# Kernel tuning notes

Hardware: AMD Instinct MI355X
Metric: run time of the kernel (lower is better)

## Reference

```python
import jax, jax.numpy as jnp
import numpy as np

B = 256      # graphs per batch
N = 512      # nodes per graph
FEAT = 64    # num_features
H = 64       # nhid
DEG = 16     # avg degree
RATIO = 0.5  # pooling_ratio
E = B * N * DEG


def setup_inputs() -> dict:
    key = jax.random.key(0)
    ks = jax.random.split(key, 12)
    # edges constructed within each graph via offsets
    src_loc = jax.random.randint(ks[0], (B, N * DEG), 0, N)
    dst_loc = jax.random.randint(ks[1], (B, N * DEG), 0, N)
    offs = (jnp.arange(B) * N)[:, None]
    edge_src = (src_loc + offs).reshape(-1).astype(jnp.int32)
    edge_dst = (dst_loc + offs).reshape(-1).astype(jnp.int32)
    batch = jnp.repeat(jnp.arange(B, dtype=jnp.int32), N)
    x = jax.random.normal(ks[2], (B * N, FEAT), dtype=jnp.float32)
    edge_attr = jax.random.uniform(ks[3], (E,), dtype=jnp.float32) + 0.1
    s1 = 1.0 / np.sqrt(FEAT)
    s2 = 1.0 / np.sqrt(H)
    return {
        "x": x,
        "edge_attr": edge_attr,
        "W1": jax.random.normal(ks[4], (FEAT, H), jnp.float32) * s1,
        "b1": jnp.zeros((H,), jnp.float32),
        "Wp1": jax.random.normal(ks[5], (H, 1), jnp.float32) * s2,
        "bp1": jnp.zeros((1,), jnp.float32),
        "W2": jax.random.normal(ks[6], (H, H), jnp.float32) * s2,
        "b2": jnp.zeros((H,), jnp.float32),
        "Wp2": jax.random.normal(ks[7], (H, 1), jnp.float32) * s2,
        "bp2": jnp.zeros((1,), jnp.float32),
        "edge_src": edge_src,
        "edge_dst": edge_dst,
        "batch": batch,
    }


def gcn_conv(x, W, b, src, dst, ew, n):
    """PyG GCNConv: sym-normalized weighted adjacency + self-loops (weight 1)."""
    h = x @ W                                   # [n, out]
    deg = jnp.zeros((n,), x.dtype).at[dst].add(ew) + 1.0  # self-loop adds 1
    dinv = jax.lax.rsqrt(deg)
    coef = dinv[dst] * ew * dinv[src]           # [E]
    out = jnp.zeros_like(h).at[dst].add(coef[:, None] * h[src])
    out = out + h * (1.0 / deg)[:, None]        # self-loop term: deg^-0.5 * 1 * deg^-0.5
    return out + b


def sag_pool(x, src, dst, ew, Wp, bp, n_per):
    """SAGPool: score = GCNConv(x)->1, per-graph top-k, gate by tanh(score),
    filter edges (dropped edges represented by zero weight)."""
    n = x.shape[0]
    score = gcn_conv(x, Wp, bp, src, dst, ew, n)[:, 0]   # [n]
    k = int(np.ceil(RATIO * n_per))
    _, idx = jax.lax.top_k(score.reshape(B, n_per), k)   # [B, k] local indices
    perm = (idx + (jnp.arange(B) * n_per)[:, None]).reshape(-1)
    xn = x[perm] * jnp.tanh(score[perm])[:, None]        # [B*k, H]
    newid = jnp.full((n,), -1, jnp.int32).at[perm].set(
        jnp.arange(B * k, dtype=jnp.int32))
    ns, nd = newid[src], newid[dst]
    valid = (ns >= 0) & (nd >= 0)
    ew2 = jnp.where(valid, ew, 0.0)
    ns = jnp.where(valid, ns, 0)
    nd = jnp.where(valid, nd, 0)
    return xn, ns, nd, ew2, k


def readout(x, k):
    """[gmp || gap] per graph; each graph has exactly k nodes, contiguous."""
    xg = x.reshape(B, k, -1)
    return jnp.concatenate([xg.max(axis=1), xg.mean(axis=1)], axis=1)  # [B, 2H]


def reference(x, edge_attr, W1, b1, Wp1, bp1, W2, b2, Wp2, bp2,
              edge_src, edge_dst, batch):
    n0 = x.shape[0]
    h = jax.nn.relu(gcn_conv(x, W1, b1, edge_src, edge_dst, edge_attr, n0))
    h, s1, d1, w1e, k1 = sag_pool(h, edge_src, edge_dst, edge_attr, Wp1, bp1, N)
    x1 = readout(h, k1)
    h = jax.nn.relu(gcn_conv(h, W2, b2, s1, d1, w1e, B * k1))
    h, _, _, _, k2 = sag_pool(h, s1, d1, w1e, Wp2, bp2, k1)
    x2 = readout(h, k2)
    return (x1 + x2) / 2.0
```

## Files before the change

### kernel.cpp

```cpp
#include <hip/hip_runtime.h>
#include <math.h>

#define BG   256
#define NN   512
#define EPG  (NN * 16)
#define NE   (BG * EPG)
#define N0   (BG * NN)
#define K1   256
#define N1_  (BG * K1)
#define K2   128
#define N2_  (BG * K2)

__device__ __forceinline__ float4 f4fma(float s, float4 a, float4 c) {
    c.x = fmaf(s, a.x, c.x); c.y = fmaf(s, a.y, c.y);
    c.z = fmaf(s, a.z, c.z); c.w = fmaf(s, a.w, c.w);
    return c;
}

template <int NPG, bool REMAP>
__global__ __launch_bounds__(512)
void stage_head_kernel(const int* __restrict__ esrc, const int* __restrict__ edst,
                       const float* __restrict__ eatt, const int* __restrict__ nid,
                       int2* __restrict__ pairs, int* __restrict__ rowstart,
                       int* __restrict__ rowcnt, float* __restrict__ dinv,
                       const float4* __restrict__ X4, const float4* __restrict__ W4,
                       float4* __restrict__ Y4, int nrows, int mmb) {
    __shared__ __align__(16) char smem[52224];
    if ((int)blockIdx.x < BG) {
        int2*  lpair = (int2*)smem;
        int*   cnt   = (int*)(smem + 32768);
        float* wsum  = (float*)(smem + 32768) + NPG;
        int*   scn   = (int*)(smem + 32768) + 2 * NPG;
        float* sdinv = (float*)(smem + 32768) + 3 * NPG;
        int*   wtot  = (int*)(smem + 32768) + 4 * NPG;
        int g = blockIdx.x;
        int e0 = g * EPG, nbase = g * NPG;
        for (int ii = threadIdx.x; ii < NPG; ii += 512) { cnt[ii] = 0; wsum[ii] = 0.f; }
        __syncthreads();
        const int4*   edst4 = (const int4*)(edst + e0);
        const int4*   esrc4 = (const int4*)(esrc + e0);
        const float4* eatt4 = (const float4*)(eatt + e0);
        int ed[16]; int es[16]; float ea[16];
#pragma unroll
        for (int c = 0; c < 4; ++c) {
            int ch = threadIdx.x + c * 512;
            int4   dd = edst4[ch];
            int4   ss = esrc4[ch];
            float4 ww = eatt4[ch];
            ed[c * 4 + 0] = dd.x; ed[c * 4 + 1] = dd.y; ed[c * 4 + 2] = dd.z; ed[c * 4 + 3] = dd.w;
            es[c * 4 + 0] = ss.x; es[c * 4 + 1] = ss.y; es[c * 4 + 2] = ss.z; es[c * 4 + 3] = ss.w;
            ea[c * 4 + 0] = ww.x; ea[c * 4 + 1] = ww.y; ea[c * 4 + 2] = ww.z; ea[c * 4 + 3] = ww.w;
        }
        if (REMAP) {
#pragma unroll
            for (int j = 0; j < 16; ++j) { ed[j] = nid[ed[j]]; es[j] = nid[es[j]]; }
        }
#pragma unroll
        for (int j = 0; j < 16; ++j) {
            bool valid = !REMAP || (ed[j] >= 0 && es[j] >= 0);
            if (valid) {
                int dl = ed[j] - nbase;
                atomicAdd(&cnt[dl], 1);
                atomicAdd(&wsum[dl], ea[j]);
            }
        }
        __syncthreads();
        int i = threadIdx.x;
        int lane = i & 63, wvid = i >> 6;
        int xval = (i < NPG) ? cnt[i] : 0;
        int xs = xval;
#pragma unroll
        for (int off = 1; off < 64; off <<= 1) {
            int v = __shfl_up(xs, off, 64);
            if (lane >= off) xs += v;
        }
        if (lane == 63) wtot[wvid] = xs;
        __syncthreads();
        int woff = 0, total = 0;
#pragma unroll
        for (int t = 0; t < 8; ++t) {
            int wt = wtot[t];
            if (t < wvid) woff += wt;
            total += wt;
        }
        xs += woff;
        if (i < NPG) {
            int st = xs - xval;
            rowstart[nbase + i] = e0 + st;
            rowcnt[nbase + i]   = xval;
            float di = rsqrtf(wsum[i] + 1.0f);
            dinv[nbase + i] = di;
            sdinv[i] = di;
            scn[i] = st;
        }
        __syncthreads();
        int slots[16]; float cf[16];
#pragma unroll
        for (int j = 0; j < 16; ++j) {
            bool valid = !REMAP || (ed[j] >= 0 && es[j] >= 0);
            slots[j] = -1;
            if (valid) {
                int dl = ed[j] - nbase, sl = es[j] - nbase;
                cf[j] = sdinv[dl] * ea[j] * sdinv[sl];
                slots[j] = atomicAdd(&scn[dl], 1);
            }
        }
#pragma unroll
        for (int j = 0; j < 16; ++j)
            if (slots[j] >= 0 && slots[j] < 4096)
                lpair[slots[j]] = make_int2(es[j] - nbase, __float_as_int(cf[j]));
        __syncthreads();
        int n0 = total < 4096 ? total : 4096;
        for (int k = threadIdx.x; k < n0; k += 512) pairs[e0 + k] = lpair[k];
        __syncthreads();
        if (total > 4096) {
#pragma unroll
            for (int j = 0; j < 16; ++j)
                if (slots[j] >= 4096)
                    lpair[slots[j] - 4096] = make_int2(es[j] - nbase, __float_as_int(cf[j]));
            __syncthreads();
            int n1 = total - 4096;
            for (int k = threadIdx.x; k < n1; k += 512) pairs[e0 + 4096 + k] = lpair[k];
        }
    } else {
        float (*sW)[68] = (float (*)[68])smem;
        int p = threadIdx.x >> 8;
        int t = threadIdx.x & 255;
        float (*sX)[68] = (float (*)[68])(smem + 17408 + p * 17408);
#pragma unroll
        for (int u = 0; u < 2; ++u) {
            int idx = threadIdx.x + u * 512;
            int r = idx >> 4, c4 = idx & 15;
            *(float4*)&sW[r][c4 * 4] = W4[idx];
        }
        int mb = blockIdx.x - BG;
        int ntiles = nrows >> 6;
        int rg = t >> 4, cg = t & 15;
        for (int tile = mb * 2 + p; tile < ntiles; tile += mmb * 2) {
            __syncthreads();
            int row0 = tile << 6;
#pragma unroll
            for (int u = 0; u < 4; ++u) {
                int idx = t + u * 256;
                int r = idx >> 4, c4 = idx & 15;
                *(float4*)&sX[r][c4 * 4] = X4[(size_t)(row0 + r) * 16 + c4];
            }
            __syncthreads();
            float4 acc0 = make_float4(0.f, 0.f, 0.f, 0.f);
            float4 acc1 = acc0, acc2 = acc0, acc3 = acc0;
#pragma unroll
            for (int k4 = 0; k4 < 16; ++k4) {
                float4 xv0 = *(const float4*)&sX[rg * 4 + 0][k4 * 4];
                float4 xv1 = *(const float4*)&sX[rg * 4 + 1][k4 * 4];
                float4 xv2 = *(const float4*)&sX[rg * 4 + 2][k4 * 4];
                float4 xv3 = *(const float4*)&sX[rg * 4 + 3][k4 * 4];
                float4 wv0 = *(const float4*)&sW[k4 * 4 + 0][cg * 4];
                float4 wv1 = *(const float4*)&sW[k4 * 4 + 1][cg * 4];
                float4 wv2 = *(const float4*)&sW[k4 * 4 + 2][cg * 4];
                float4 wv3 = *(const float4*)&sW[k4 * 4 + 3][cg * 4];
                acc0 = f4fma(xv0.x, wv0, acc0); acc0 = f4fma(xv0.y, wv1, acc0);
                acc0 = f4fma(xv0.z, wv2, acc0); acc0 = f4fma(xv0.w, wv3, acc0);
                acc1 = f4fma(xv1.x, wv0, acc1); acc1 = f4fma(xv1.y, wv1, acc1);
                acc1 = f4fma(xv1.z, wv2, acc1); acc1 = f4fma(xv1.w, wv3, acc1);
                acc2 = f4fma(xv2.x, wv0, acc2); acc2 = f4fma(xv2.y, wv1, acc2);
                acc2 = f4fma(xv2.z, wv2, acc2); acc2 = f4fma(xv2.w, wv3, acc2);
                acc3 = f4fma(xv3.x, wv0, acc3); acc3 = f4fma(xv3.y, wv1, acc3);
                acc3 = f4fma(xv3.z, wv2, acc3); acc3 = f4fma(xv3.w, wv3, acc3);
            }
            size_t ob = (size_t)(row0 + rg * 4) * 16 + cg;
            Y4[ob]      = acc0;
            Y4[ob + 16] = acc1;
            Y4[ob + 32] = acc2;
            Y4[ob + 48] = acc3;
        }
    }
}

template <int NPG, int K, bool FINAL>
__global__ __launch_bounds__(512)
void tail_kernel(const float4* __restrict__ hx4, const int2* __restrict__ pairs,
                 const int* __restrict__ rowstart, const int* __restrict__ rowcnt,
                 const float* __restrict__ dinv, const float4* __restrict__ b4,
                 const float4* __restrict__ wp4, const float* __restrict__ bp,
                 int* __restrict__ nid, float4* __restrict__ xn4,
                 float* __restrict__ xr, const float* __restrict__ x1r,
                 float* __restrict__ out) {
    constexpr int PASSES = NPG / 32;
    constexpr int SH_A  = NPG * 68;
    constexpr int SH_UN = 4096;
    __shared__ __align__(16) float smem[SH_A + SH_UN + 2 * NPG + 64 + 64];
    float*  shx  = smem;
    int*    perm = (int*)(smem + SH_A);
    float*  shp  = smem + SH_A + NPG;
    float4* smx  = (float4*)(smem + SH_A);
    float4* ssm  = (float4*)(smem + SH_A + 2048);
    float*  ssc  = smem + SH_A + SH_UN;
    int*    rnk  = (int*)(smem + SH_A + SH_UN + NPG);
    float*  sbw  = smem + SH_A + SH_UN + 2 * NPG;
    int*    hist = (int*)(smem + SH_A + SH_UN + 2 * NPG + 64);

    int g = blockIdx.x, nbase = g * NPG;
    int t = threadIdx.x;
    int lane16 = t & 15, sub = (t >> 4) & 3, wv = t >> 6, lane = t & 63;

    for (int i = t; i < NPG * 16; i += 512) {
        int r = i >> 4, c4 = i & 15;
        *(float4*)&shx[r * 68 + c4 * 4] = hx4[(size_t)nbase * 16 + i];
    }
    if (t < 64) { sbw[t] = ((const float*)b4)[t]; hist[t] = 0; }
    __syncthreads();
    for (int i = t; i < NPG; i += 512) {
        int c = min(rowcnt[nbase + i], 63);
        atomicAdd(&hist[c], 1);
    }
    __syncthreads();
    if (t < 64) {
        int v = hist[t], s = v;
#pragma unroll
        for (int off = 1; off < 64; off <<= 1) {
            int u = __shfl_up(s, off, 64);
            if (lane >= off) s += u;
        }
        hist[t] = s - v;
    }
    __syncthreads();
    for (int i = t; i < NPG; i += 512) {
        int c = min(rowcnt[nbase + i], 63);
        int pos = atomicAdd(&hist[c], 1);
        perm[pos] = i;
    }
    __syncthreads();
    int idx = wv * 64 + lane;
    float4 acc[16];
    int nl = 0;
    if (idx < NPG) {
        nl = perm[idx];
        int st = rowstart[nbase + nl], cn = rowcnt[nbase + nl];
        float di = dinv[nbase + nl], dii = di * di;
#pragma unroll
        for (int c = 0; c < 16; ++c) {
            float4 xv = *(const float4*)&shx[nl * 68 + c * 4];
            acc[c].x = fmaf(xv.x, dii, sbw[c * 4 + 0]);
            acc[c].y = fmaf(xv.y, dii, sbw[c * 4 + 1]);
            acc[c].z = fmaf(xv.z, dii, sbw[c * 4 + 2]);
            acc[c].w = fmaf(xv.w, dii, sbw[c * 4 + 3]);
        }
        int2 pc = (cn > 0) ? pairs[st] : make_int2(0, 0);
        for (int j = 0; j < cn; ++j) {
            int2 pn = (j + 1 < cn) ? pairs[st + j + 1] : make_int2(0, 0);
            float cf = __int_as_float(pc.y);
            int   s  = pc.x;
#pragma unroll
            for (int c = 0; c < 16; ++c)
                acc[c] = f4fma(cf, *(const float4*)&shx[s * 68 + c * 4], acc[c]);
            pc = pn;
        }
#pragma unroll
        for (int c = 0; c < 16; ++c) {
            acc[c].x = fmaxf(acc[c].x, 0.f); acc[c].y = fmaxf(acc[c].y, 0.f);
            acc[c].z = fmaxf(acc[c].z, 0.f); acc[c].w = fmaxf(acc[c].w, 0.f);
        }
    }
    __syncthreads();
    if (idx < NPG) {
#pragma unroll
        for (int c = 0; c < 16; ++c)
            *(float4*)&shx[nl * 68 + c * 4] = acc[c];
    }
    __syncthreads();
    float4 w4 = wp4[lane16];
#pragma unroll
    for (int p = 0; p < PASSES; ++p) {
        int n2 = p * 32 + wv * 4 + sub;
        float4 a = *(const float4*)&shx[n2 * 68 + lane16 * 4];
        float tt = a.x * w4.x + a.y * w4.y + a.z * w4.z + a.w * w4.w;
        tt += __shfl_xor(tt, 1, 64); tt += __shfl_xor(tt, 2, 64);
        tt += __shfl_xor(tt, 4, 64); tt += __shfl_xor(tt, 8, 64);
        if (lane16 == 0) shp[n2] = tt;
    }
    __syncthreads();
    if (t < NPG) {
        int i = perm[t];
        int st = rowstart[nbase + i], cn = rowcnt[nbase + i];
        float di = dinv[nbase + i];
        float a = fmaf(shp[i], di * di, bp[0]);
        for (int j = 0; j < cn; ++j) {
            int2 pr = pairs[st + j];
            a = fmaf(__int_as_float(pr.y), shp[pr.x], a);
        }
        ssc[i] = a;
    }
    __syncthreads();
    for (int i = t; i < NPG; i += 512) {
        float si = ssc[i];
        int rank = 0;
        for (int j = 0; j < NPG; ++j) {
            float sj = ssc[j];
            rank += (sj > si) || (sj == si && j < i);
        }
        rnk[i] = rank;
        if (!FINAL) nid[nbase + i] = (rank < K) ? (g * K + rank) : -1;
    }
    __syncthreads();
    float4 mx = make_float4(-3.402823466e38f, -3.402823466e38f, -3.402823466e38f, -3.402823466e38f);
    float4 sm = make_float4(0.f, 0.f, 0.f, 0.f);
#pragma unroll
    for (int p = 0; p < PASSES; ++p) {
        int n2 = p * 32 + wv * 4 + sub;
        int r = rnk[n2];
        if (r < K) {
            float gt = tanhf(ssc[n2]);
            float4 v = *(const float4*)&shx[n2 * 68 + lane16 * 4];
            v.x *= gt; v.y *= gt; v.z *= gt; v.w *= gt;
            if (!FINAL) xn4[((size_t)g * K + r) * 16 + lane16] = v;
            mx.x = fmaxf(mx.x, v.x); mx.y = fmaxf(mx.y, v.y);
            mx.z = fmaxf(mx.z, v.z); mx.w = fmaxf(mx.w, v.w);
            sm.x += v.x; sm.y += v.y; sm.z += v.z; sm.w += v.w;
        }
    }
    int grp = t >> 4;
    __syncthreads();
    smx[grp * 16 + lane16] = mx;
    ssm[grp * 16 + lane16] = sm;
    __syncthreads();
    if (grp == 0) {
#pragma unroll
        for (int u = 1; u < 32; ++u) {
            float4 a = smx[u * 16 + lane16], b = ssm[u * 16 + lane16];
            mx.x = fmaxf(mx.x, a.x); mx.y = fmaxf(mx.y, a.y);
            mx.z = fmaxf(mx.z, a.z); mx.w = fmaxf(mx.w, a.w);
            sm.x += b.x; sm.y += b.y; sm.z += b.z; sm.w += b.w;
        }
        float invK = 1.f / K;
        int c = lane16 * 4;
        float mr[4] = {mx.x, mx.y, mx.z, mx.w};
        float ar[4] = {sm.x * invK, sm.y * invK, sm.z * invK, sm.w * invK};
#pragma unroll
        for (int u = 0; u < 4; ++u) {
            if (FINAL) {
                out[g * 128 + c + u]      = 0.5f * (x1r[g * 128 + c + u]      + mr[u]);
                out[g * 128 + 64 + c + u] = 0.5f * (x1r[g * 128 + 64 + c + u] + ar[u]);
            } else {
                xr[g * 128 + c + u]      = mr[u];
                xr[g * 128 + 64 + c + u] = ar[u];
            }
        }
    }
}

extern "C" void kernel_launch(void* const* d_in, const int* in_sizes, int n_in,
                              void* d_out, int out_size, void* d_ws, size_t ws_size,
                              hipStream_t stream) {
    const float* x    = (const float*)d_in[0];
    const float* eatt = (const float*)d_in[1];
    const float* W1   = (const float*)d_in[2];
    const float* b1   = (const float*)d_in[3];
    const float* Wp1  = (const float*)d_in[4];
    const float* bp1  = (const float*)d_in[5];
    const float* W2   = (const float*)d_in[6];
    const float* b2   = (const float*)d_in[7];
    const float* Wp2  = (const float*)d_in[8];
    const float* bp2  = (const float*)d_in[9];
    const int*   esrc = (const int*)d_in[10];
    const int*   edst = (const int*)d_in[11];
    float* out = (float*)d_out;

    float* ws = (float*)d_ws;
    size_t o = 0;
    float* A    = ws + o; o += (size_t)N0 * 64;
    float* xn1  = ws + o; o += (size_t)N1_ * 64;
    int2*  prs  = (int2*)(ws + o); o += (size_t)NE * 2;
    int*   rst  = (int*)(ws + o); o += N0;
    int*   rcn  = (int*)(ws + o); o += N0;
    float* dinv = ws + o; o += N0;
    int*   nid  = (int*)(ws + o); o += N0;
    float* x1r  = ws + o; o += BG * 128;

    float* hx1 = A;
    float* hx2 = A;

    stage_head_kernel<NN, false><<<BG + 512, 512, 0, stream>>>(
        esrc, edst, eatt, nullptr, prs, rst, rcn, dinv,
        (const float4*)x, (const float4*)W1, (float4*)hx1, N0, 512);
    tail_kernel<NN, K1, false><<<BG, 512, 0, stream>>>(
        (const float4*)hx1, prs, rst, rcn, dinv, (const float4*)b1,
        (const float4*)Wp1, bp1, nid, (float4*)xn1, x1r, nullptr, nullptr);
    stage_head_kernel<K1, true><<<BG + 256, 512, 0, stream>>>(
        esrc, edst, eatt, nid, prs, rst, rcn, dinv,
        (const float4*)xn1, (const float4*)W2, (float4*)hx2, N1_, 256);
    tail_kernel<K1, K2, true><<<BG, 512, 0, stream>>>(
        (const float4*)hx2, prs, rst, rcn, dinv, (const float4*)b2,
        (const float4*)Wp2, bp2, nullptr, nullptr, nullptr, x1r, out);
}
```

Baseline: 224.5 us.

## Double tail kernel block to 1024 threads, splitting aggregation and ranking work

The tail kernel now runs 1024 threads per graph. The neighbor aggregation splits each node's 64 features across 2 or 4 threads, which cuts per-thread accumulator registers. The O(N^2) top-k rank computation is split across thread partitions using float4 reads, with the partial ranks combined by shared atomics. A deeper edge-pair prefetch is added. The cost is more threads competing for LDS and more barriers, with half the threads idle in the score and readout phases.

```diff
diff --git a/kernel.cpp b/kernel.cpp
--- a/kernel.cpp
+++ b/kernel.cpp
@@ -177,7 +177,7 @@
 }
 
 template <int NPG, int K, bool FINAL>
-__global__ __launch_bounds__(512)
+__global__ __launch_bounds__(1024)
 void tail_kernel(const float4* __restrict__ hx4, const int2* __restrict__ pairs,
                  const int* __restrict__ rowstart, const int* __restrict__ rowcnt,
                  const float* __restrict__ dinv, const float4* __restrict__ b4,
@@ -186,6 +186,11 @@
                  float* __restrict__ xr, const float* __restrict__ x1r,
                  float* __restrict__ out) {
     constexpr int PASSES = NPG / 32;
+    constexpr int LPN = 1024 / NPG;
+    constexpr int LOG_LPN = (LPN == 2) ? 1 : 2;
+    constexpr int QF = 16 / LPN;
+    constexpr int RLOG = (NPG == 512) ? 9 : 8;
+    constexpr int RCH = NPG * NPG / 1024;
     constexpr int SH_A  = NPG * 68;
     constexpr int SH_UN = 4096;
     __shared__ __align__(16) float smem[SH_A + SH_UN + 2 * NPG + 64 + 64];
@@ -201,15 +206,16 @@
 
     int g = blockIdx.x, nbase = g * NPG;
     int t = threadIdx.x;
-    int lane16 = t & 15, sub = (t >> 4) & 3, wv = t >> 6, lane = t & 63;
-
-    for (int i = t; i < NPG * 16; i += 512) {
+    int lane16 = t & 15, lane = t & 63;
+
+    for (int i = t; i < NPG * 16; i += 1024) {
         int r = i >> 4, c4 = i & 15;
         *(float4*)&shx[r * 68 + c4 * 4] = hx4[(size_t)nbase * 16 + i];
     }
     if (t < 64) { sbw[t] = ((const float*)b4)[t]; hist[t] = 0; }
-    __syncthreads();
-    for (int i = t; i < NPG; i += 512) {
+    for (int i = t; i < NPG; i += 1024) rnk[i] = 0;
+    __syncthreads();
+    for (int i = t; i < NPG; i += 1024) {
         int c = min(rowcnt[nbase + i], 63);
         atomicAdd(&hist[c], 1);
     }
@@ -224,59 +230,62 @@
         hist[t] = s - v;
     }
     __syncthreads();
-    for (int i = t; i < NPG; i += 512) {
+    for (int i = t; i < NPG; i += 1024) {
         int c = min(rowcnt[nbase + i], 63);
         int pos = atomicAdd(&hist[c], 1);
         perm[pos] = i;
     }
     __syncthreads();
-    int idx = wv * 64 + lane;
-    float4 acc[16];
-    int nl = 0;
-    if (idx < NPG) {
-        nl = perm[idx];
+    {
+        int idx2 = t >> LOG_LPN;
+        int half = t & (LPN - 1);
+        int nl = perm[idx2];
         int st = rowstart[nbase + nl], cn = rowcnt[nbase + nl];
         float di = dinv[nbase + nl], dii = di * di;
-#pragma unroll
-        for (int c = 0; c < 16; ++c) {
-            float4 xv = *(const float4*)&shx[nl * 68 + c * 4];
-            acc[c].x = fmaf(xv.x, dii, sbw[c * 4 + 0]);
-            acc[c].y = fmaf(xv.y, dii, sbw[c * 4 + 1]);
-            acc[c].z = fmaf(xv.z, dii, sbw[c * 4 + 2]);
-            acc[c].w = fmaf(xv.w, dii, sbw[c * 4 + 3]);
-        }
-        int2 pc = (cn > 0) ? pairs[st] : make_int2(0, 0);
+        int fb = half * QF;
+        float4 acc[QF];
+#pragma unroll
+        for (int c = 0; c < QF; ++c) {
+            float4 xv = *(const float4*)&shx[nl * 68 + (fb + c) * 4];
+            acc[c].x = fmaf(xv.x, dii, sbw[(fb + c) * 4 + 0]);
+            acc[c].y = fmaf(xv.y, dii, sbw[(fb + c) * 4 + 1]);
+            acc[c].z = fmaf(xv.z, dii, sbw[(fb + c) * 4 + 2]);
+            acc[c].w = fmaf(xv.w, dii, sbw[(fb + c) * 4 + 3]);
+        }
+        int2 p0 = (cn > 0) ? pairs[st] : make_int2(0, 0);
+        int2 p1 = (cn > 1) ? pairs[st + 1] : make_int2(0, 0);
         for (int j = 0; j < cn; ++j) {
-            int2 pn = (j + 1 < cn) ? pairs[st + j + 1] : make_int2(0, 0);
-            float cf = __int_as_float(pc.y);
-            int   s  = pc.x;
-#pragma unroll
-            for (int c = 0; c < 16; ++c)
-                acc[c] = f4fma(cf, *(const float4*)&shx[s * 68 + c * 4], acc[c]);
-            pc = pn;
-        }
-#pragma unroll
-        for (int c = 0; c < 16; ++c) {
+            int2 p2 = (j + 2 < cn) ? pairs[st + j + 2] : make_int2(0, 0);
+            float cf = __int_as_float(p0.y);
+            int   s  = p0.x;
+#pragma unroll
+            for (int c = 0; c < QF; ++c)
+                acc[c] = f4fma(cf, *(const float4*)&shx[s * 68 + (fb + c) * 4], acc[c]);
+            p0 = p1; p1 = p2;
+        }
+#pragma unroll
+        for (int c = 0; c < QF; ++c) {
             acc[c].x = fmaxf(acc[c].x, 0.f); acc[c].y = fmaxf(acc[c].y, 0.f);
             acc[c].z = fmaxf(acc[c].z, 0.f); acc[c].w = fmaxf(acc[c].w, 0.f);
         }
-    }
-    __syncthreads();
-    if (idx < NPG) {
-#pragma unroll
-        for (int c = 0; c < 16; ++c)
-            *(float4*)&shx[nl * 68 + c * 4] = acc[c];
-    }
-    __syncthreads();
-    float4 w4 = wp4[lane16];
-#pragma unroll
-    for (int p = 0; p < PASSES; ++p) {
-        int n2 = p * 32 + wv * 4 + sub;
-        float4 a = *(const float4*)&shx[n2 * 68 + lane16 * 4];
-        float tt = a.x * w4.x + a.y * w4.y + a.z * w4.z + a.w * w4.w;
-        tt += __shfl_xor(tt, 1, 64); tt += __shfl_xor(tt, 2, 64);
-        tt += __shfl_xor(tt, 4, 64); tt += __shfl_xor(tt, 8, 64);
-        if (lane16 == 0) shp[n2] = tt;
+        __syncthreads();
+#pragma unroll
+        for (int c = 0; c < QF; ++c)
+            *(float4*)&shx[nl * 68 + (fb + c) * 4] = acc[c];
+    }
+    __syncthreads();
+    if (t < 512) {
+        int wv8 = t >> 6, sub4 = (t >> 4) & 3;
+        float4 w4 = wp4[lane16];
+#pragma unroll
+        for (int p = 0; p < PASSES; ++p) {
+            int n2 = p * 32 + wv8 * 4 + sub4;
+            float4 a = *(const float4*)&shx[n2 * 68 + lane16 * 4];
+            float tt = a.x * w4.x + a.y * w4.y + a.z * w4.z + a.w * w4.w;
+            tt += __shfl_xor(tt, 1, 64); tt += __shfl_xor(tt, 2, 64);
+            tt += __shfl_xor(tt, 4, 64); tt += __shfl_xor(tt, 8, 64);
+            if (lane16 == 0) shp[n2] = tt;
+        }
     }
     __syncthreads();
     if (t < NPG) {
@@ -284,44 +293,60 @@
         int st = rowstart[nbase + i], cn = rowcnt[nbase + i];
         float di = dinv[nbase + i];
         float a = fmaf(shp[i], di * di, bp[0]);
+        int2 q0 = (cn > 0) ? pairs[st] : make_int2(0, 0);
+        int2 q1 = (cn > 1) ? pairs[st + 1] : make_int2(0, 0);
         for (int j = 0; j < cn; ++j) {
-            int2 pr = pairs[st + j];
-            a = fmaf(__int_as_float(pr.y), shp[pr.x], a);
+            int2 q2 = (j + 2 < cn) ? pairs[st + j + 2] : make_int2(0, 0);
+            a = fmaf(__int_as_float(q0.y), shp[q0.x], a);
+            q0 = q1; q1 = q2;
         }
         ssc[i] = a;
     }
     __syncthreads();
-    for (int i = t; i < NPG; i += 512) {
+    {
+        int part = t >> RLOG;
+        int i = t & (NPG - 1);
         float si = ssc[i];
+        int j0 = part * RCH;
         int rank = 0;
-        for (int j = 0; j < NPG; ++j) {
-            float sj = ssc[j];
-            rank += (sj > si) || (sj == si && j < i);
-        }
-        rnk[i] = rank;
-        if (!FINAL) nid[nbase + i] = (rank < K) ? (g * K + rank) : -1;
-    }
-    __syncthreads();
+        for (int j = j0; j < j0 + RCH; j += 4) {
+            float4 sj = *(const float4*)&ssc[j];
+            rank += (sj.x > si) || (sj.x == si && j     < i);
+            rank += (sj.y > si) || (sj.y == si && j + 1 < i);
+            rank += (sj.z > si) || (sj.z == si && j + 2 < i);
+            rank += (sj.w > si) || (sj.w == si && j + 3 < i);
+        }
+        atomicAdd(&rnk[i], rank);
+    }
+    __syncthreads();
+    if (!FINAL)
+        for (int i = t; i < NPG; i += 1024)
+            nid[nbase + i] = (rnk[i] < K) ? (g * K + rnk[i]) : -1;
     float4 mx = make_float4(-3.402823466e38f, -3.402823466e38f, -3.402823466e38f, -3.402823466e38f);
     float4 sm = make_float4(0.f, 0.f, 0.f, 0.f);
-#pragma unroll
-    for (int p = 0; p < PASSES; ++p) {
-        int n2 = p * 32 + wv * 4 + sub;
-        int r = rnk[n2];
-        if (r < K) {
-            float gt = tanhf(ssc[n2]);
-            float4 v = *(const float4*)&shx[n2 * 68 + lane16 * 4];
-            v.x *= gt; v.y *= gt; v.z *= gt; v.w *= gt;
-            if (!FINAL) xn4[((size_t)g * K + r) * 16 + lane16] = v;
-            mx.x = fmaxf(mx.x, v.x); mx.y = fmaxf(mx.y, v.y);
-            mx.z = fmaxf(mx.z, v.z); mx.w = fmaxf(mx.w, v.w);
-            sm.x += v.x; sm.y += v.y; sm.z += v.z; sm.w += v.w;
+    if (t < 512) {
+        int wv8 = t >> 6, sub4 = (t >> 4) & 3;
+#pragma unroll
+        for (int p = 0; p < PASSES; ++p) {
+            int n2 = p * 32 + wv8 * 4 + sub4;
+            int r = rnk[n2];
+            if (r < K) {
+                float gt = tanhf(ssc[n2]);
+                float4 v = *(const float4*)&shx[n2 * 68 + lane16 * 4];
+                v.x *= gt; v.y *= gt; v.z *= gt; v.w *= gt;
+                if (!FINAL) xn4[((size_t)g * K + r) * 16 + lane16] = v;
+                mx.x = fmaxf(mx.x, v.x); mx.y = fmaxf(mx.y, v.y);
+                mx.z = fmaxf(mx.z, v.z); mx.w = fmaxf(mx.w, v.w);
+                sm.x += v.x; sm.y += v.y; sm.z += v.z; sm.w += v.w;
+            }
         }
     }
     int grp = t >> 4;
     __syncthreads();
-    smx[grp * 16 + lane16] = mx;
-    ssm[grp * 16 + lane16] = sm;
+    if (t < 512) {
+        smx[grp * 16 + lane16] = mx;
+        ssm[grp * 16 + lane16] = sm;
+    }
     __syncthreads();
     if (grp == 0) {
 #pragma unroll
@@ -382,13 +407,13 @@
     stage_head_kernel<NN, false><<<BG + 512, 512, 0, stream>>>(
         esrc, edst, eatt, nullptr, prs, rst, rcn, dinv,
         (const float4*)x, (const float4*)W1, (float4*)hx1, N0, 512);
-    tail_kernel<NN, K1, false><<<BG, 512, 0, stream>>>(
+    tail_kernel<NN, K1, false><<<BG, 1024, 0, stream>>>(
         (const float4*)hx1, prs, rst, rcn, dinv, (const float4*)b1,
         (const float4*)Wp1, bp1, nid, (float4*)xn1, x1r, nullptr, nullptr);
     stage_head_kernel<K1, true><<<BG + 256, 512, 0, stream>>>(
         esrc, edst, eatt, nid, prs, rst, rcn, dinv,
         (const float4*)xn1, (const float4*)W2, (float4*)hx2, N1_, 256);
-    tail_kernel<K1, K2, true><<<BG, 512, 0, stream>>>(
+    tail_kernel<K1, K2, true><<<BG, 1024, 0, stream>>>(
         (const float4*)hx2, prs, rst, rcn, dinv, (const float4*)b2,
         (const float4*)Wp2, bp2, nullptr, nullptr, nullptr, x1r, out);
 }
```

New measurement: 218.1 us. 1.03x faster.
